# Performance work log

Measured on AMD Instinct MI355X. Metric: run time of the kernel, lower is better.

## Reference

```python
import jax, jax.numpy as jnp
import numpy as np

D_MODEL = 1024
N_HEADS = 16
HEAD_DIM = D_MODEL // N_HEADS
ROPE_THETA = 10000.0


def _rope_cache(seq_len, head_dim, dtype, theta=ROPE_THETA):
    half = head_dim // 2
    inv_freq = 1.0 / theta ** (jnp.arange(half, dtype=jnp.float32) / half)
    t = jnp.arange(seq_len, dtype=jnp.float32)
    freqs = jnp.outer(t, inv_freq)                 # [L, half]
    emb = jnp.concatenate([freqs, freqs], axis=-1)  # [L, head_dim]
    return jnp.cos(emb).astype(dtype), jnp.sin(emb).astype(dtype)


def _rotate_half(x):
    d = x.shape[-1]
    x1, x2 = x[..., : d // 2], x[..., d // 2 :]
    return jnp.concatenate([-x2, x1], axis=-1)


def _apply_rope(x, cos, sin):
    return x * cos + _rotate_half(x) * sin


def setup_inputs() -> dict:
    key = jax.random.key(0)
    ks = jax.random.split(key, 9)
    B, L, D = 2, 2048, D_MODEL
    s = 1.0 / np.sqrt(D)
    return {
        "x": jax.random.normal(ks[0], (B, L, D), dtype=jnp.float32),
        "Wq": jax.random.normal(ks[1], (D, D), dtype=jnp.float32) * s,
        "bq": jnp.zeros((D,), dtype=jnp.float32),
        "Wk": jax.random.normal(ks[2], (D, D), dtype=jnp.float32) * s,
        "bk": jnp.zeros((D,), dtype=jnp.float32),
        "Wv": jax.random.normal(ks[3], (D, D), dtype=jnp.float32) * s,
        "bv": jnp.zeros((D,), dtype=jnp.float32),
        "Wo": jax.random.normal(ks[4], (D, D), dtype=jnp.float32) * s,
        "bo": jnp.zeros((D,), dtype=jnp.float32),
    }


def reference(x, Wq, bq, Wk, bk, Wv, bv, Wo, bo):
    B, L, D = x.shape
    H, Hd = N_HEADS, HEAD_DIM
    scale = Hd ** -0.5

    def proj(W, b):
        # [B,L,D] -> [B,H,L,Hd]
        return (x @ W.T + b).reshape(B, L, H, Hd).transpose(0, 2, 1, 3)

    q = proj(Wq, bq)
    k = proj(Wk, bk)
    v = proj(Wv, bv)

    cos, sin = _rope_cache(L, Hd, x.dtype)  # [L, Hd]
    q = _apply_rope(q, cos, sin)
    k = _apply_rope(k, cos, sin)

    scores = jnp.einsum("bhqd,bhkd->bhqk", q, k) * scale  # [B,H,L,L]
    attn = jax.nn.softmax(scores, axis=-1)
    ctx = jnp.einsum("bhqk,bhkd->bhqd", attn, v)           # [B,H,L,Hd]
    ctx = ctx.transpose(0, 2, 1, 3).reshape(B, L, D)
    return ctx @ Wo.T + bo
```

## Files before the change

kernel.cpp:

```cpp
#include <hip/hip_runtime.h>

typedef unsigned short u16;
typedef unsigned int u32;
typedef __attribute__((ext_vector_type(8))) __bf16 bf16v8;
typedef __attribute__((ext_vector_type(4))) __bf16 bf16v4;
typedef __attribute__((ext_vector_type(4))) float f32x4;
typedef __attribute__((ext_vector_type(16))) float f32x16;
typedef __attribute__((ext_vector_type(2))) unsigned u32x2;

#define SEQ    2048
#define NBATCH 2
#define NHEAD  16
#define HD     64
#define DM     1024
#define MROWS  4096

__device__ __forceinline__ u16 f2bf(float f) {
  unsigned int u = __float_as_uint(f);
  u += 0x7FFFu + ((u >> 16) & 1u);
  return (u16)(u >> 16);
}

__device__ __forceinline__ void gll16(const void* g, void* l) {
  __builtin_amdgcn_global_load_lds(
      (__attribute__((address_space(1))) void*)g,
      (__attribute__((address_space(3))) void*)l, 16, 0, 0);
}

__global__ __launch_bounds__(256) void k_prep(
    const float* __restrict__ x,
    const float* __restrict__ Wq, const float* __restrict__ Wk,
    const float* __restrict__ Wv, const float* __restrict__ Wo,
    u16* __restrict__ Xb, u16* __restrict__ Wqb, u16* __restrict__ Wkb,
    u16* __restrict__ Wvb, u16* __restrict__ Wob,
    float* __restrict__ cosT, float* __restrict__ sinT) {
  int bid = blockIdx.x;
  if (bid < MROWS * DM / 1024) {
    int i = bid * 256 + threadIdx.x;
    float4 v = ((const float4*)x)[i];
    ushort4 o;
    o.x = f2bf(v.x); o.y = f2bf(v.y); o.z = f2bf(v.z); o.w = f2bf(v.w);
    ((ushort4*)Xb)[i] = o;
    return;
  }
  bid -= MROWS * DM / 1024;
  if (bid < 4 * (DM * DM / 1024)) {
    int seg = bid >> 10;
    int i = (bid & 1023) * 256 + threadIdx.x;
    const float* src = (seg == 0) ? Wq : (seg == 1) ? Wk : (seg == 2) ? Wv : Wo;
    u16* dst = (seg == 0) ? Wqb : (seg == 1) ? Wkb : (seg == 2) ? Wvb : Wob;
    float4 v = ((const float4*)src)[i];
    ushort4 o;
    o.x = f2bf(v.x); o.y = f2bf(v.y); o.z = f2bf(v.z); o.w = f2bf(v.w);
    ((ushort4*)dst)[i] = o;
    return;
  }
  bid -= 4 * (DM * DM / 1024);
  int idx = bid * 256 + threadIdx.x;
  int l = idx >> 5, d = idx & 31;
  float inv = 1.0f / powf(10000.0f, (float)d * (1.0f / 32.0f));
  float ang = (float)l * inv;
  float s, c;
  sincosf(ang, &s, &c);
  cosT[idx] = c;
  sinT[idx] = s;
}

__global__ __launch_bounds__(256) void k_gemm_qkv(
    const u16* __restrict__ A,
    const u16* W0, const u16* W1, const u16* W2,
    const float* b0, const float* b1, const float* b2,
    u16* __restrict__ Qr, u16* __restrict__ Kg, u16* __restrict__ Vg,
    const float* __restrict__ cosT, const float* __restrict__ sinT) {
  __shared__ __attribute__((aligned(16))) u16 As[128 * 64];
  __shared__ __attribute__((aligned(16))) u16 Bs[128 * 64];
  const int z = blockIdx.z;
  const u16* W = (z == 0) ? W0 : ((z == 1) ? W1 : W2);
  const float* bias = (z == 0) ? b0 : ((z == 1) ? b1 : b2);

  const int tid = threadIdx.x;
  const int lane = tid & 63, wid = tid >> 6;
  const int g = lane >> 4, c = lane & 15;
  const int wm = wid >> 1, wn = wid & 1;
  const int bm = blockIdx.x, bn = blockIdx.y;

  const f32x4 vz = {0.f, 0.f, 0.f, 0.f};
  f32x4 acc[4][4];
#pragma unroll
  for (int i = 0; i < 4; i++)
#pragma unroll
    for (int j = 0; j < 4; j++) acc[i][j] = vz;

  const int srow = tid >> 3;
  const int scb = tid & 7;

  for (int kt = 0; kt < DM / 64; ++kt) {
    __syncthreads();
#pragma unroll
    for (int cc = 0; cc < 4; ++cc) {
      int row = cc * 32 + srow;
      int sc = scb ^ (row & 7);
      gll16(A + (size_t)(bm * 128 + row) * DM + kt * 64 + sc * 8,
            &As[cc * 2048 + wid * 512]);
      gll16(W + (size_t)(bn * 128 + row) * DM + kt * 64 + sc * 8,
            &Bs[cc * 2048 + wid * 512]);
    }
    __syncthreads();
#pragma unroll
    for (int kk = 0; kk < 2; ++kk) {
      bf16v8 av[4], bv[4];
#pragma unroll
      for (int i = 0; i < 4; i++) {
        int row = wm * 64 + i * 16 + c;
        int sc = (kk * 4 + g) ^ (row & 7);
        av[i] = *(const bf16v8*)&As[row * 64 + sc * 8];
      }
#pragma unroll
      for (int j = 0; j < 4; j++) {
        int row = wn * 64 + j * 16 + c;
        int sc = (kk * 4 + g) ^ (row & 7);
        bv[j] = *(const bf16v8*)&Bs[row * 64 + sc * 8];
      }
#pragma unroll
      for (int i = 0; i < 4; i++)
#pragma unroll
        for (int j = 0; j < 4; j++)
          acc[i][j] = __builtin_amdgcn_mfma_f32_16x16x32_bf16(av[i], bv[j], acc[i][j], 0, 0, 0);
    }
  }

  if (z == 2) {
    const int h = bn * 2 + wn;
#pragma unroll
    for (int i = 0; i < 4; i++) {
      int m0 = bm * 128 + wm * 64 + i * 16 + g * 4;
#pragma unroll
      for (int r = 0; r < 4; r++) {
        int m = m0 + r;
        int tok = m & (SEQ - 1);
        int b = m >> 11;
        size_t base = ((size_t)((b * NHEAD + h) * 256 + (tok >> 3)) * 64) * 8 + (tok & 7);
#pragma unroll
        for (int j = 0; j < 4; j++) {
          int d = j * 16 + c;
          Vg[base + (size_t)d * 8] = f2bf(acc[i][j][r] + bias[bn * 128 + wn * 64 + d]);
        }
      }
    }
  } else if (z == 1) {
    const int h = bn * 2 + wn;
    const int nb = bn * 128 + wn * 64;
#pragma unroll
    for (int i = 0; i < 4; i++) {
      int m0 = bm * 128 + wm * 64 + i * 16 + g * 4;
#pragma unroll
      for (int r = 0; r < 4; r++) {
        int m = m0 + r;
        int tok = m & (SEQ - 1);
        int b = m >> 11;
        size_t bhb = (size_t)(b * NHEAD + h) * 8;
#pragma unroll
        for (int j = 0; j < 2; j++) {
          int d = j * 16 + c;
          float x1 = acc[i][j][r] + bias[nb + d];
          float x2 = acc[i][j + 2][r] + bias[nb + d + 32];
          float cs = cosT[tok * 32 + d];
          float sn = sinT[tok * 32 + d];
          Kg[(bhb + (d >> 3)) * (SEQ * 8) + tok * 8 + (d & 7)]     = f2bf(x1 * cs - x2 * sn);
          Kg[(bhb + 4 + (d >> 3)) * (SEQ * 8) + tok * 8 + (d & 7)] = f2bf(x2 * cs + x1 * sn);
        }
      }
    }
  } else {
    const float qs = 0.180336880f;
    const int h = bn * 2 + wn;
    const int nb = bn * 128 + wn * 64;
#pragma unroll
    for (int i = 0; i < 4; i++) {
      int m0 = bm * 128 + wm * 64 + i * 16 + g * 4;
#pragma unroll
      for (int r = 0; r < 4; r++) {
        int m = m0 + r;
        int tok = m & (SEQ - 1);
        int b = m >> 11;
        size_t obase = ((size_t)(b * NHEAD + h) * SEQ + tok) * HD;
#pragma unroll
        for (int j = 0; j < 2; j++) {
          int d = j * 16 + c;
          float x1 = acc[i][j][r] + bias[nb + d];
          float x2 = acc[i][j + 2][r] + bias[nb + d + 32];
          float cs = cosT[tok * 32 + d];
          float sn = sinT[tok * 32 + d];
          Qr[obase + d]      = f2bf((x1 * cs - x2 * sn) * qs);
          Qr[obase + d + 32] = f2bf((x2 * cs + x1 * sn) * qs);
        }
      }
    }
  }
}

__global__ __launch_bounds__(256) void k_gemm_out(
    const u16* __restrict__ A, const u16* __restrict__ W,
    const float* __restrict__ bias, float* __restrict__ out) {
  __shared__ __attribute__((aligned(16))) u16 As[128 * 64];
  __shared__ __attribute__((aligned(16))) u16 Bs[128 * 64];
  const int tid = threadIdx.x;
  const int lane = tid & 63, wid = tid >> 6;
  const int g = lane >> 4, c = lane & 15;
  const int wm = wid >> 1, wn = wid & 1;
  const int bm = blockIdx.x, bn = blockIdx.y;

  const f32x4 vz = {0.f, 0.f, 0.f, 0.f};
  f32x4 acc[4][4];
#pragma unroll
  for (int i = 0; i < 4; i++)
#pragma unroll
    for (int j = 0; j < 4; j++) acc[i][j] = vz;

  const int srow = tid >> 3;
  const int scb = tid & 7;

  for (int kt = 0; kt < DM / 64; ++kt) {
    __syncthreads();
#pragma unroll
    for (int cc = 0; cc < 4; ++cc) {
      int row = cc * 32 + srow;
      int sc = scb ^ (row & 7);
      gll16(A + (size_t)(bm * 128 + row) * DM + kt * 64 + sc * 8,
            &As[cc * 2048 + wid * 512]);
      gll16(W + (size_t)(bn * 128 + row) * DM + kt * 64 + sc * 8,
            &Bs[cc * 2048 + wid * 512]);
    }
    __syncthreads();
#pragma unroll
    for (int kk = 0; kk < 2; ++kk) {
      bf16v8 av[4], bv[4];
#pragma unroll
      for (int i = 0; i < 4; i++) {
        int row = wm * 64 + i * 16 + c;
        int sc = (kk * 4 + g) ^ (row & 7);
        av[i] = *(const bf16v8*)&As[row * 64 + sc * 8];
      }
#pragma unroll
      for (int j = 0; j < 4; j++) {
        int row = wn * 64 + j * 16 + c;
        int sc = (kk * 4 + g) ^ (row & 7);
        bv[j] = *(const bf16v8*)&Bs[row * 64 + sc * 8];
      }
#pragma unroll
      for (int i = 0; i < 4; i++)
#pragma unroll
        for (int j = 0; j < 4; j++)
          acc[i][j] = __builtin_amdgcn_mfma_f32_16x16x32_bf16(av[i], bv[j], acc[i][j], 0, 0, 0);
    }
  }

#pragma unroll
  for (int i = 0; i < 4; i++) {
    int m = bm * 128 + wm * 64 + i * 16 + g * 4;
#pragma unroll
    for (int j = 0; j < 4; j++) {
      int n = bn * 128 + wn * 64 + j * 16 + c;
      float bb = bias[n];
#pragma unroll
      for (int r = 0; r < 4; r++)
        out[(size_t)(m + r) * DM + n] = acc[i][j][r] + bb;
    }
  }
}

__global__ __launch_bounds__(256, 2) void k_attn(
    const u16* __restrict__ Qb, const u16* __restrict__ Kg,
    const u16* __restrict__ Vg, u16* __restrict__ Cb) {
  __shared__ __attribute__((aligned(16))) u16 Ks[2][8 * 64 * 8];
  __shared__ __attribute__((aligned(16))) u16 Vs[2][8 * 64 * 8];
  const int tid = threadIdx.x, lane = tid & 63, wid = tid >> 6;
  const int hh = lane >> 5, ln = lane & 31;
  const int bh = blockIdx.y;
  const int q0 = blockIdx.x * 128 + wid * 32;

  const u16* Qh = Qb + ((size_t)bh * SEQ + q0 + ln) * HD + hh * 8;
  bf16v8 qf[4];
#pragma unroll
  for (int ks = 0; ks < 4; ks++) qf[ks] = *(const bf16v8*)(Qh + ks * 16);

  f32x16 octx[2];
#pragma unroll
  for (int dsub = 0; dsub < 2; dsub++)
#pragma unroll
    for (int r = 0; r < 16; r++) octx[dsub][r] = 0.f;
  float lacc = 0.f;

#define STAGE(buf, kv0)                                                              \
  {                                                                                  \
    _Pragma("unroll") for (int cc = 0; cc < 2; ++cc) {                               \
      int kk = wid * 2 + cc;                                                         \
      gll16(Kg + ((size_t)(bh * 8 + kk) * SEQ + (kv0)) * 8 + lane * 8,               \
            &Ks[buf][kk * 512]);                                                     \
      gll16(Vg + ((size_t)(bh * 256 + ((kv0) >> 3) + kk) * 64 + lane) * 8,           \
            &Vs[buf][kk * 512]);                                                     \
    }                                                                                \
  }

  STAGE(0, 0);
  __syncthreads();
  int cur = 0;

  for (int kv = 0; kv < SEQ / 64; ++kv) {
    if (kv + 1 < SEQ / 64) STAGE(cur ^ 1, (kv + 1) * 64);
    const u16* Kc = Ks[cur];
    const u16* Vc = Vs[cur];

    bf16v8 pb[4];
#pragma unroll
    for (int s = 0; s < 2; s++) {
      f32x16 sT;
#pragma unroll
      for (int r = 0; r < 16; r++) sT[r] = 0.f;
#pragma unroll
      for (int ks = 0; ks < 4; ks++) {
        bf16v8 kf = *(const bf16v8*)&Kc[(ks * 2 + hh) * 512 + (s * 32 + ln) * 8];
        sT = __builtin_amdgcn_mfma_f32_32x32x16_bf16(kf, qf[ks], sT, 0, 0, 0);
      }
      float p[16];
#pragma unroll
      for (int r = 0; r < 16; r++) {
        p[r] = __builtin_amdgcn_exp2f(sT[r]);
        lacc += p[r];
      }
#pragma unroll
      for (int ksl = 0; ksl < 2; ksl++) {
        const int bb = ksl * 8;
        u32 Aw, Bw, Cw, Dw;
        asm("v_cvt_pk_bf16_f32 %0, %1, %2" : "=v"(Aw) : "v"(p[bb + 0]), "v"(p[bb + 1]));
        asm("v_cvt_pk_bf16_f32 %0, %1, %2" : "=v"(Bw) : "v"(p[bb + 2]), "v"(p[bb + 3]));
        asm("v_cvt_pk_bf16_f32 %0, %1, %2" : "=v"(Cw) : "v"(p[bb + 4]), "v"(p[bb + 5]));
        asm("v_cvt_pk_bf16_f32 %0, %1, %2" : "=v"(Dw) : "v"(p[bb + 6]), "v"(p[bb + 7]));
        u32x2 r02 = __builtin_amdgcn_permlane32_swap(Aw, Cw, false, false);
        u32x2 r13 = __builtin_amdgcn_permlane32_swap(Bw, Dw, false, false);
        union { u32 w[4]; bf16v8 v; } pu;
        pu.w[0] = r02[0]; pu.w[1] = r13[0]; pu.w[2] = r02[1]; pu.w[3] = r13[1];
        pb[s * 2 + ksl] = pu.v;
      }
    }

#pragma unroll
    for (int dsub = 0; dsub < 2; dsub++)
#pragma unroll
      for (int ks = 0; ks < 4; ks++) {
        bf16v8 vf = *(const bf16v8*)&Vc[(ks * 2 + hh) * 512 + (dsub * 32 + ln) * 8];
        octx[dsub] = __builtin_amdgcn_mfma_f32_32x32x16_bf16(vf, pb[ks], octx[dsub], 0, 0, 0);
      }

    __syncthreads();
    cur ^= 1;
  }

  float lt = lacc + __shfl_xor(lacc, 32);
  float inv = 1.0f / lt;

  const int b = bh >> 4, h = bh & 15;
  const int q = q0 + ln;
  u16* orow = Cb + ((size_t)(b * SEQ + q)) * DM + h * HD;
#pragma unroll
  for (int dsub = 0; dsub < 2; dsub++)
#pragma unroll
    for (int rr = 0; rr < 4; rr++) {
      int d0 = dsub * 32 + rr * 8 + hh * 4;
      bf16v4 o4 = {(__bf16)(octx[dsub][rr * 4 + 0] * inv),
                   (__bf16)(octx[dsub][rr * 4 + 1] * inv),
                   (__bf16)(octx[dsub][rr * 4 + 2] * inv),
                   (__bf16)(octx[dsub][rr * 4 + 3] * inv)};
      *(bf16v4*)(orow + d0) = o4;
    }
}

extern "C" void kernel_launch(void* const* d_in, const int* in_sizes, int n_in,
                              void* d_out, int out_size, void* d_ws, size_t ws_size,
                              hipStream_t stream) {
  (void)in_sizes; (void)n_in; (void)out_size;
  const float* x  = (const float*)d_in[0];
  const float* Wq = (const float*)d_in[1];
  const float* bq = (const float*)d_in[2];
  const float* Wk = (const float*)d_in[3];
  const float* bk = (const float*)d_in[4];
  const float* Wv = (const float*)d_in[5];
  const float* bv = (const float*)d_in[6];
  const float* Wo = (const float*)d_in[7];
  const float* bo = (const float*)d_in[8];
  float* out = (float*)d_out;
  char* ws = (char*)d_ws;
  const size_t MB = 1024ull * 1024ull;

  if (ws_size < 49ull * MB) return;

  float* cosT = (float*)(ws);
  float* sinT = (float*)(ws + 256 * 1024);
  u16* Xb  = (u16*)(ws + 512 * 1024);
  u16* Wqb = (u16*)(ws + 512 * 1024 + 8 * MB);
  u16* Wkb = (u16*)(ws + 512 * 1024 + 10 * MB);
  u16* Wvb = (u16*)(ws + 512 * 1024 + 12 * MB);
  u16* Wob = (u16*)(ws + 512 * 1024 + 14 * MB);
  u16* Qr  = (u16*)(ws + 512 * 1024 + 24 * MB);
  u16* Kg  = (u16*)(ws + 512 * 1024 + 32 * MB);
  u16* Vg  = (u16*)(ws + 512 * 1024 + 40 * MB);
  u16* Cb  = Xb;

  k_prep<<<dim3(8448), 256, 0, stream>>>(x, Wq, Wk, Wv, Wo, Xb, Wqb, Wkb, Wvb, Wob,
                                         cosT, sinT);

  dim3 gp(MROWS / 128, DM / 128, 3);
  k_gemm_qkv<<<gp, 256, 0, stream>>>(Xb, Wqb, Wkb, Wvb, bq, bk, bv, Qr, Kg, Vg,
                                     cosT, sinT);

  dim3 ga(SEQ / 128, NBATCH * NHEAD);
  k_attn<<<ga, 256, 0, stream>>>(Qr, Kg, Vg, Cb);

  dim3 go(MROWS / 128, DM / 128);
  k_gemm_out<<<go, 256, 0, stream>>>(Cb, Wob, bo, out);
}
```

Measured before the change: 122.4 us.

## Split attention KV range across two wave teams per block and merge via LDS

The attention kernel now launches 512 threads per block, with two teams of four waves each handling half of the KV sequence for the same 128 queries. Partial context accumulators and row sums from the second team are written to shared memory and combined by the first team before normalization and store. The row-sum accumulator is also split into four lanes to shorten the dependency chain. This doubles the waves per block to improve latency hiding. In exchange it uses 64KB of LDS per block, adds a reduction step with extra barriers, and raises the occupancy target to four blocks of 512 threads.

```diff
diff --git a/kernel.cpp b/kernel.cpp
--- a/kernel.cpp
+++ b/kernel.cpp
@@ -269,15 +269,15 @@
   }
 }
 
-__global__ __launch_bounds__(256, 2) void k_attn(
+__global__ __launch_bounds__(512, 4) void k_attn(
     const u16* __restrict__ Qb, const u16* __restrict__ Kg,
     const u16* __restrict__ Vg, u16* __restrict__ Cb) {
-  __shared__ __attribute__((aligned(16))) u16 Ks[2][8 * 64 * 8];
-  __shared__ __attribute__((aligned(16))) u16 Vs[2][8 * 64 * 8];
+  __shared__ __attribute__((aligned(16))) u16 SMEM[32768];
   const int tid = threadIdx.x, lane = tid & 63, wid = tid >> 6;
   const int hh = lane >> 5, ln = lane & 31;
+  const int team = wid >> 2, lw = wid & 3;
   const int bh = blockIdx.y;
-  const int q0 = blockIdx.x * 128 + wid * 32;
+  const int q0 = blockIdx.x * 128 + lw * 32;
 
   const u16* Qh = Qb + ((size_t)bh * SEQ + q0 + ln) * HD + hh * 8;
   bf16v8 qf[4];
@@ -289,27 +289,31 @@
   for (int dsub = 0; dsub < 2; dsub++)
 #pragma unroll
     for (int r = 0; r < 16; r++) octx[dsub][r] = 0.f;
-  float lacc = 0.f;
+  f32x4 lac4 = {0.f, 0.f, 0.f, 0.f};
+
+  const int kvbase = team * 1024;
 
 #define STAGE(buf, kv0)                                                              \
   {                                                                                  \
+    u16* Kb_ = &SMEM[(team * 2 + (buf)) * 8192];                                     \
+    u16* Vb_ = Kb_ + 4096;                                                           \
     _Pragma("unroll") for (int cc = 0; cc < 2; ++cc) {                               \
-      int kk = wid * 2 + cc;                                                         \
+      int kk = lw * 2 + cc;                                                          \
       gll16(Kg + ((size_t)(bh * 8 + kk) * SEQ + (kv0)) * 8 + lane * 8,               \
-            &Ks[buf][kk * 512]);                                                     \
+            &Kb_[kk * 512]);                                                         \
       gll16(Vg + ((size_t)(bh * 256 + ((kv0) >> 3) + kk) * 64 + lane) * 8,           \
-            &Vs[buf][kk * 512]);                                                     \
+            &Vb_[kk * 512]);                                                         \
     }                                                                                \
   }
 
-  STAGE(0, 0);
+  STAGE(0, kvbase);
   __syncthreads();
   int cur = 0;
 
-  for (int kv = 0; kv < SEQ / 64; ++kv) {
-    if (kv + 1 < SEQ / 64) STAGE(cur ^ 1, (kv + 1) * 64);
-    const u16* Kc = Ks[cur];
-    const u16* Vc = Vs[cur];
+  for (int it = 0; it < 16; ++it) {
+    if (it + 1 < 16) STAGE(cur ^ 1, kvbase + (it + 1) * 64);
+    const u16* Kc = &SMEM[(team * 2 + cur) * 8192];
+    const u16* Vc = Kc + 4096;
 
     bf16v8 pb[4];
 #pragma unroll
@@ -326,7 +330,7 @@
 #pragma unroll
       for (int r = 0; r < 16; r++) {
         p[r] = __builtin_amdgcn_exp2f(sT[r]);
-        lacc += p[r];
+        lac4[r & 3] += p[r];
       }
 #pragma unroll
       for (int ksl = 0; ksl < 2; ksl++) {
@@ -356,23 +360,43 @@
     cur ^= 1;
   }
 
-  float lt = lacc + __shfl_xor(lacc, 32);
-  float inv = 1.0f / lt;
-
-  const int b = bh >> 4, h = bh & 15;
-  const int q = q0 + ln;
-  u16* orow = Cb + ((size_t)(b * SEQ + q)) * DM + h * HD;
-#pragma unroll
-  for (int dsub = 0; dsub < 2; dsub++)
-#pragma unroll
-    for (int rr = 0; rr < 4; rr++) {
-      int d0 = dsub * 32 + rr * 8 + hh * 4;
-      bf16v4 o4 = {(__bf16)(octx[dsub][rr * 4 + 0] * inv),
-                   (__bf16)(octx[dsub][rr * 4 + 1] * inv),
-                   (__bf16)(octx[dsub][rr * 4 + 2] * inv),
-                   (__bf16)(octx[dsub][rr * 4 + 3] * inv)};
-      *(bf16v4*)(orow + d0) = o4;
-    }
+  float lacc = (lac4[0] + lac4[1]) + (lac4[2] + lac4[3]);
+  float lt_own = lacc + __shfl_xor(lacc, 32);
+
+  float* Mo = (float*)SMEM;
+  float* Ml = ((float*)SMEM) + 8192;
+  __syncthreads();
+  if (team == 1) {
+#pragma unroll
+    for (int dsub = 0; dsub < 2; dsub++)
+#pragma unroll
+      for (int rr = 0; rr < 4; rr++) {
+        f32x4 v = {octx[dsub][rr * 4 + 0], octx[dsub][rr * 4 + 1],
+                   octx[dsub][rr * 4 + 2], octx[dsub][rr * 4 + 3]};
+        *(f32x4*)&Mo[(((lw * 8) + dsub * 4 + rr) * 64 + lane) * 4] = v;
+      }
+    if (hh == 0) Ml[lw * 32 + ln] = lt_own;
+  }
+  __syncthreads();
+  if (team == 0) {
+    float lt = lt_own + Ml[lw * 32 + ln];
+    float inv = 1.0f / lt;
+    const int b = bh >> 4, h = bh & 15;
+    const int q = q0 + ln;
+    u16* orow = Cb + ((size_t)(b * SEQ + q)) * DM + h * HD;
+#pragma unroll
+    for (int dsub = 0; dsub < 2; dsub++)
+#pragma unroll
+      for (int rr = 0; rr < 4; rr++) {
+        f32x4 m = *(const f32x4*)&Mo[(((lw * 8) + dsub * 4 + rr) * 64 + lane) * 4];
+        int d0 = dsub * 32 + rr * 8 + hh * 4;
+        bf16v4 o4 = {(__bf16)((octx[dsub][rr * 4 + 0] + m[0]) * inv),
+                     (__bf16)((octx[dsub][rr * 4 + 1] + m[1]) * inv),
+                     (__bf16)((octx[dsub][rr * 4 + 2] + m[2]) * inv),
+                     (__bf16)((octx[dsub][rr * 4 + 3] + m[3]) * inv)};
+        *(bf16v4*)(orow + d0) = o4;
+      }
+  }
 }
 
 extern "C" void kernel_launch(void* const* d_in, const int* in_sizes, int n_in,
@@ -414,7 +438,7 @@
                                      cosT, sinT);
 
   dim3 ga(SEQ / 128, NBATCH * NHEAD);
-  k_attn<<<ga, 256, 0, stream>>>(Qr, Kg, Vg, Cb);
+  k_attn<<<ga, 512, 0, stream>>>(Qr, Kg, Vg, Cb);
 
   dim3 go(MROWS / 128, DM / 128);
   k_gemm_out<<<go, 256, 0, stream>>>(Cb, Wob, bo, out);
```

New measurement: 117.9 us. -3.7%, faster.
